# Optimization experiments

Hardware: AMD Instinct MI355X
Metric: run time of the kernel (lower is better)

Reference implementation:

```python
import jax, jax.numpy as jnp
import numpy as np

N, NC, E = 100000, 50000, 1600000   # source points, centers, edges
D, P, H, O = 64, 3, 128, 128        # feat dim, pos dim, hidden, out


def setup_inputs() -> dict:
    key = jax.random.key(0)
    ks = jax.random.split(key, 10)
    x = jax.random.normal(ks[0], (N, D), jnp.float32)
    x_c = jax.random.normal(ks[1], (NC, O), jnp.float32)  # only shape is used
    pos = jax.random.normal(ks[2], (N, P), jnp.float32)
    pos_c = jax.random.normal(ks[3], (NC, P), jnp.float32)
    src = jax.random.randint(ks[4], (E,), 0, N)
    dst = jax.random.randint(ks[5], (E,), 0, NC)
    W1 = jax.random.normal(ks[6], (D + P, H), jnp.float32) / jnp.sqrt(D + P)
    b1 = jnp.zeros((H,), jnp.float32)
    W2 = jax.random.normal(ks[7], (H, O), jnp.float32) / jnp.sqrt(H)
    b2 = jnp.zeros((O,), jnp.float32)
    return dict(x=x, x_c=x_c, pos=pos, pos_c=pos_c, src=src, dst=dst,
                W1=W1, b1=b1, W2=W2, b2=b2)


def reference(x, x_c, pos, pos_c, src, dst, W1, b1, W2, b2):
    # gather per-edge features: [E, D+P]
    feats = jnp.concatenate([x[src], pos[src] - pos_c[dst]], axis=1)
    # MLP on edges
    h = jax.nn.relu(feats @ W1 + b1) @ W2 + b2  # [E, O]
    # scatter-max aggregation onto centers
    agg = jax.ops.segment_max(h, dst, num_segments=x_c.shape[0])  # [NC, O]
    # match torch_scatter convention: empty segments -> 0 (not -inf)
    return jnp.where(jnp.isneginf(agg), 0.0, agg)
```

## Files before the change

### kernel.cpp

```cpp
#include <hip/hip_runtime.h>
#include <hip/hip_bf16.h>

#define NPTS   100000
#define NCENT  50000
#define NEDGE  1600000
#define DF     64
#define DP     3
#define DH     128
#define DOUT   128
#define TILE   128
#define LDA    104
#define LDH    136
#define LDF    66
#define NCPAD  50176

typedef __attribute__((ext_vector_type(8))) short short8;
typedef __attribute__((ext_vector_type(4))) float f32x4;

__device__ __forceinline__ unsigned short f2bf(float f) {
  union { __hip_bfloat16 h; unsigned short u; } v;
  v.h = __float2bfloat16(f);
  return v.u;
}

__device__ __forceinline__ unsigned encodeKey(float f) {
  unsigned u = __float_as_uint(f);
  return u ^ ((unsigned)((int)u >> 31) | 0x80000000u);
}

__device__ __forceinline__ float decodeKey(unsigned k) {
  if (k == 0u) return 0.0f;
  unsigned u = (k & 0x80000000u) ? (k ^ 0x80000000u) : ~k;
  return __uint_as_float(u);
}

__global__ void k_prep(const float* __restrict__ x, const float* __restrict__ W1,
                       const float* __restrict__ W2, unsigned short* __restrict__ xbf,
                       unsigned short* __restrict__ W1f, unsigned short* __restrict__ W2f,
                       int* __restrict__ cnt, unsigned* __restrict__ outU) {
  const int b = blockIdx.x;
  const int t = threadIdx.x;
  if (b < 6250) {
    int i = b * 256 + t;
    reinterpret_cast<uint4*>(outU)[i] = make_uint4(0u, 0u, 0u, 0u);
  } else if (b < 9375) {
    int i = (b - 6250) * 256 + t;
    const float4* xr = reinterpret_cast<const float4*>(x);
    float4 v0 = xr[2 * i], v1 = xr[2 * i + 1];
    short8 w;
    w[0] = (short)f2bf(v0.x); w[1] = (short)f2bf(v0.y);
    w[2] = (short)f2bf(v0.z); w[3] = (short)f2bf(v0.w);
    w[4] = (short)f2bf(v1.x); w[5] = (short)f2bf(v1.y);
    w[6] = (short)f2bf(v1.z); w[7] = (short)f2bf(v1.w);
    reinterpret_cast<short8*>(xbf)[i] = w;
  } else if (b < 9571) {
    cnt[(b - 9375) * 256 + t] = 0;
  } else if (b < 9577) {
    int tid = (b - 9571) * 256 + t;
    int lane = tid & 63, g = tid >> 6;
    int nt = g / 3, ks = g % 3;
    int n = nt * 16 + (lane & 15);
    int k0 = ks * 32 + (lane >> 4) * 8;
    short8 v;
    for (int j = 0; j < 8; ++j) {
      int k = k0 + j;
      float f = (k < DF + DP) ? W1[k * DH + n] : 0.0f;
      v[j] = (short)f2bf(f);
    }
    *reinterpret_cast<short8*>(W1f + (size_t)tid * 8) = v;
  } else {
    int tid = (b - 9577) * 256 + t;
    int lane = tid & 63, g = tid >> 6;
    int nt = g >> 2, ks = g & 3;
    int n = nt * 16 + (lane & 15);
    int k0 = ks * 32 + (lane >> 4) * 8;
    short8 v;
    for (int j = 0; j < 8; ++j) {
      int k = k0 + j;
      v[j] = (short)f2bf(W2[k * DH + n]);
    }
    *reinterpret_cast<short8*>(W2f + (size_t)tid * 8) = v;
  }
}


__global__ void k_rank(const int* __restrict__ dst, int* __restrict__ cnt,
                       int* __restrict__ rank) {
  int i = blockIdx.x * 256 + threadIdx.x;
  rank[i] = atomicAdd(&cnt[dst[i]], 1);
}

__global__ void k_s1(const int* __restrict__ cnt, int* __restrict__ bsum) {
  __shared__ int sh[256];
  int t = threadIdx.x;
  sh[t] = cnt[blockIdx.x * 256 + t];
  __syncthreads();
  for (int off = 128; off > 0; off >>= 1) {
    if (t < off) sh[t] += sh[t + off];
    __syncthreads();
  }
  if (t == 0) bsum[blockIdx.x] = sh[0];
}

__global__ void k_s2(const int* __restrict__ bsum, int* __restrict__ bbase) {
  __shared__ int sh[256];
  int t = threadIdx.x;
  int v = (t < 196) ? bsum[t] : 0;
  sh[t] = v;
  __syncthreads();
  for (int off = 1; off < 256; off <<= 1) {
    int u = (t >= off) ? sh[t - off] : 0;
    __syncthreads();
    sh[t] += u;
    __syncthreads();
  }
  if (t < 196) bbase[t] = sh[t] - v;
}

__global__ void k_s3(int* __restrict__ cnt, const int* __restrict__ bbase) {
  __shared__ int sh[256];
  int t = threadIdx.x, i = blockIdx.x * 256 + t;
  int v = cnt[i];
  sh[t] = v;
  __syncthreads();
  for (int off = 1; off < 256; off <<= 1) {
    int u = (t >= off) ? sh[t - off] : 0;
    __syncthreads();
    sh[t] += u;
    __syncthreads();
  }
  cnt[i] = sh[t] - v + bbase[blockIdx.x];
}

__global__ void k_place(const int* __restrict__ src, const int* __restrict__ dst,
                        const int* __restrict__ base, const int* __restrict__ rank,
                        unsigned long long* __restrict__ sdS) {
  int i = blockIdx.x * 256 + threadIdx.x;
  int d = dst[i];
  int p = base[d] + rank[i];
  sdS[p] = ((unsigned long long)(unsigned)d << 32) | (unsigned)src[i];
}

__global__ void k_decode(unsigned* __restrict__ out) {
  int i = blockIdx.x * blockDim.x + threadIdx.x;
  uint4 v = reinterpret_cast<uint4*>(out)[i];
  float4 f;
  f.x = decodeKey(v.x);
  f.y = decodeKey(v.y);
  f.z = decodeKey(v.z);
  f.w = decodeKey(v.w);
  reinterpret_cast<float4*>(out)[i] = f;
}

__global__ void __launch_bounds__(256, 4)
k_mlp(const unsigned short* __restrict__ xbf, const float* __restrict__ pos,
      const float* __restrict__ pos_c, const unsigned long long* __restrict__ sdS,
      const float* __restrict__ b1, const float* __restrict__ b2,
      const unsigned short* __restrict__ W1f, const unsigned short* __restrict__ W2f,
      unsigned* __restrict__ outU) {
  __shared__ __align__(16) unsigned short buf[TILE * LDH];
  __shared__ int dstLoc[TILE];

  const int t = threadIdx.x;
  const int e0 = blockIdx.x * TILE;

  {
    const int e = t >> 1, p = t & 1;
    const unsigned long long rec = sdS[e0 + e];
    const int s = (int)(rec & 0xffffffffu);
    const short8* xr = reinterpret_cast<const short8*>(xbf + (size_t)s * DF);
    for (int i = 0; i < 4; ++i)
      *reinterpret_cast<short8*>(&buf[e * LDA + p * 32 + i * 8]) = xr[p * 4 + i];
    short8 z = {0, 0, 0, 0, 0, 0, 0, 0};
    *reinterpret_cast<short8*>(&buf[e * LDA + 72 + p * 16]) = z;
    *reinterpret_cast<short8*>(&buf[e * LDA + 72 + p * 16 + 8]) = z;
  }
  if (t < TILE) {
    const unsigned long long rec = sdS[e0 + t];
    const int s = (int)(rec & 0xffffffffu);
    const int c = (int)(rec >> 32);
    dstLoc[t] = c;
    float dx = pos[(size_t)s * 3 + 0] - pos_c[(size_t)c * 3 + 0];
    float dy = pos[(size_t)s * 3 + 1] - pos_c[(size_t)c * 3 + 1];
    float dz = pos[(size_t)s * 3 + 2] - pos_c[(size_t)c * 3 + 2];
    short8 w = {0, 0, 0, 0, 0, 0, 0, 0};
    w[0] = (short)f2bf(dx); w[1] = (short)f2bf(dy); w[2] = (short)f2bf(dz);
    *reinterpret_cast<short8*>(&buf[t * LDA + 64]) = w;
  }
  __syncthreads();

  const int lane = t & 63;
  const int w = t >> 6;
  const int l16 = lane & 15;
  const int quad = lane >> 4;

  short8 a1[2][3];
  for (int mi = 0; mi < 2; ++mi) {
    int row = (2 * w + mi) * 16 + l16;
    for (int ks = 0; ks < 3; ++ks)
      a1[mi][ks] = *reinterpret_cast<const short8*>(&buf[row * LDA + ks * 32 + quad * 8]);
  }
  __syncthreads();

  for (int nt = 0; nt < 8; ++nt) {
    short8 b[3];
    for (int ks = 0; ks < 3; ++ks)
      b[ks] = *reinterpret_cast<const short8*>(W1f + ((size_t)(nt * 3 + ks) * 64 + lane) * 8);
    f32x4 acc0 = {0.f, 0.f, 0.f, 0.f}, acc1 = {0.f, 0.f, 0.f, 0.f};
    for (int ks = 0; ks < 3; ++ks) {
      acc0 = __builtin_amdgcn_mfma_f32_16x16x32_bf16(a1[0][ks], b[ks], acc0, 0, 0, 0);
      acc1 = __builtin_amdgcn_mfma_f32_16x16x32_bf16(a1[1][ks], b[ks], acc1, 0, 0, 0);
    }
    int n = nt * 16 + l16;
    float bias = b1[n];
    for (int r = 0; r < 4; ++r) {
      float v0 = acc0[r] + bias; v0 = v0 > 0.f ? v0 : 0.f;
      buf[((2 * w) * 16 + quad * 4 + r) * LDH + n] = f2bf(v0);
      float v1 = acc1[r] + bias; v1 = v1 > 0.f ? v1 : 0.f;
      buf[((2 * w + 1) * 16 + quad * 4 + r) * LDH + n] = f2bf(v1);
    }
  }
  __syncthreads();

  short8 a2[2][4];
  for (int mi = 0; mi < 2; ++mi) {
    int row = (2 * w + mi) * 16 + l16;
    for (int ks = 0; ks < 4; ++ks)
      a2[mi][ks] = *reinterpret_cast<const short8*>(&buf[row * LDH + ks * 32 + quad * 8]);
  }
  __syncthreads();

  float* Sf = reinterpret_cast<float*>(buf);
  const int col = t & 63;
  const int chunk = t >> 6;

  for (int half = 0; half < 2; ++half) {
    for (int ntl = 0; ntl < 4; ++ntl) {
      const int nt = half * 4 + ntl;
      short8 b[4];
      for (int ks = 0; ks < 4; ++ks)
        b[ks] = *reinterpret_cast<const short8*>(W2f + ((size_t)(nt * 4 + ks) * 64 + lane) * 8);
      f32x4 acc0 = {0.f, 0.f, 0.f, 0.f}, acc1 = {0.f, 0.f, 0.f, 0.f};
      for (int ks = 0; ks < 4; ++ks) {
        acc0 = __builtin_amdgcn_mfma_f32_16x16x32_bf16(a2[0][ks], b[ks], acc0, 0, 0, 0);
        acc1 = __builtin_amdgcn_mfma_f32_16x16x32_bf16(a2[1][ks], b[ks], acc1, 0, 0, 0);
      }
      const int nl = ntl * 16 + l16;
      const float bias = b2[half * 64 + nl];
      for (int r = 0; r < 4; ++r) {
        int edge0 = (2 * w) * 16 + quad * 4 + r;
        Sf[edge0 * LDF + nl] = acc0[r] + bias;
        int edge1 = (2 * w + 1) * 16 + quad * 4 + r;
        Sf[edge1 * LDF + nl] = acc1[r] + bias;
      }
    }
    __syncthreads();
    float running = -3.402823466e38f;
    int cur_d = dstLoc[chunk * 32];
    for (int i = 0; i < 32; ++i) {
      const int ei = chunk * 32 + i;
      const int d = dstLoc[ei];
      if (d != cur_d) {
        atomicMax(&outU[(size_t)cur_d * DOUT + half * 64 + col], encodeKey(running));
        running = -3.402823466e38f;
        cur_d = d;
      }
      running = fmaxf(running, Sf[ei * LDF + col]);
    }
    atomicMax(&outU[(size_t)cur_d * DOUT + half * 64 + col], encodeKey(running));
    __syncthreads();
  }
}

extern "C" void kernel_launch(void* const* d_in, const int* in_sizes, int n_in,
                              void* d_out, int out_size, void* d_ws, size_t ws_size,
                              hipStream_t stream) {
  const float* x     = (const float*)d_in[0];
  const float* pos   = (const float*)d_in[2];
  const float* pos_c = (const float*)d_in[3];
  const int*   src   = (const int*)d_in[4];
  const int*   dst   = (const int*)d_in[5];
  const float* W1    = (const float*)d_in[6];
  const float* b1    = (const float*)d_in[7];
  const float* W2    = (const float*)d_in[8];
  const float* b2    = (const float*)d_in[9];
  unsigned* outU = (unsigned*)d_out;

  char* base = (char*)d_ws;
  unsigned short* W1f = (unsigned short*)base;
  unsigned short* W2f = (unsigned short*)(base + 24576);
  int* bsum  = (int*)(base + 57344);
  int* bbase = (int*)(base + 58368);
  int* cnt   = (int*)(base + 65536);
  int* rank  = (int*)(base + 266240);
  unsigned long long* sdS = (unsigned long long*)(base + 6666240);
  unsigned short* xbf = (unsigned short*)(base + 19466240);

  k_prep<<<9585, 256, 0, stream>>>(x, W1, W2, xbf, W1f, W2f, cnt, outU);
  k_rank<<<NEDGE / 256, 256, 0, stream>>>(dst, cnt, rank);
  k_s1<<<NCPAD / 256, 256, 0, stream>>>(cnt, bsum);
  k_s2<<<1, 256, 0, stream>>>(bsum, bbase);
  k_s3<<<NCPAD / 256, 256, 0, stream>>>(cnt, bbase);
  k_place<<<NEDGE / 256, 256, 0, stream>>>(src, dst, cnt, rank, sdS);
  k_mlp<<<NEDGE / TILE, 256, 0, stream>>>(xbf, pos, pos_c, sdS,
                                          b1, b2, W1f, W2f, outU);
  k_decode<<<(NCENT * DOUT / 4) / 256, 256, 0, stream>>>(outU);
}
```

Baseline: 396.7 us.

## Drop rank array, fuse counting into prep, transpose scatter-max staging buffer

Removes the per-edge rank array by having k_place take slots with atomicAdd on the scanned offsets, and folds the dst histogram into k_prep. Zeroing of counts and output moves to hipMemsetAsync. In the MLP epilogue, results are stored transposed so each column thread reads its 32 edges as float4 vectors, and segment boundaries come from a precomputed ballot mask instead of reading dstLoc every edge. The order of edges within a segment becomes nondeterministic, which is harmless for max, and the transposed float4 LDS stores may cause bank conflicts.

```diff
diff --git a/kernel.cpp b/kernel.cpp
--- a/kernel.cpp
+++ b/kernel.cpp
@@ -11,7 +11,7 @@
 #define TILE   128
 #define LDA    104
 #define LDH    136
-#define LDF    66
+#define LDE    132
 #define NCPAD  50176
 
 typedef __attribute__((ext_vector_type(8))) short short8;
@@ -35,16 +35,13 @@
 }
 
 __global__ void k_prep(const float* __restrict__ x, const float* __restrict__ W1,
-                       const float* __restrict__ W2, unsigned short* __restrict__ xbf,
-                       unsigned short* __restrict__ W1f, unsigned short* __restrict__ W2f,
-                       int* __restrict__ cnt, unsigned* __restrict__ outU) {
+                       const float* __restrict__ W2, const int* __restrict__ dst,
+                       unsigned short* __restrict__ xbf, unsigned short* __restrict__ W1f,
+                       unsigned short* __restrict__ W2f, int* __restrict__ cnt) {
   const int b = blockIdx.x;
   const int t = threadIdx.x;
-  if (b < 6250) {
+  if (b < 3125) {
     int i = b * 256 + t;
-    reinterpret_cast<uint4*>(outU)[i] = make_uint4(0u, 0u, 0u, 0u);
-  } else if (b < 9375) {
-    int i = (b - 6250) * 256 + t;
     const float4* xr = reinterpret_cast<const float4*>(x);
     float4 v0 = xr[2 * i], v1 = xr[2 * i + 1];
     short8 w;
@@ -53,10 +50,8 @@
     w[4] = (short)f2bf(v1.x); w[5] = (short)f2bf(v1.y);
     w[6] = (short)f2bf(v1.z); w[7] = (short)f2bf(v1.w);
     reinterpret_cast<short8*>(xbf)[i] = w;
-  } else if (b < 9571) {
-    cnt[(b - 9375) * 256 + t] = 0;
-  } else if (b < 9577) {
-    int tid = (b - 9571) * 256 + t;
+  } else if (b < 3131) {
+    int tid = (b - 3125) * 256 + t;
     int lane = tid & 63, g = tid >> 6;
     int nt = g / 3, ks = g % 3;
     int n = nt * 16 + (lane & 15);
@@ -68,8 +63,8 @@
       v[j] = (short)f2bf(f);
     }
     *reinterpret_cast<short8*>(W1f + (size_t)tid * 8) = v;
-  } else {
-    int tid = (b - 9577) * 256 + t;
+  } else if (b < 3139) {
+    int tid = (b - 3131) * 256 + t;
     int lane = tid & 63, g = tid >> 6;
     int nt = g >> 2, ks = g & 3;
     int n = nt * 16 + (lane & 15);
@@ -80,15 +75,12 @@
       v[j] = (short)f2bf(W2[k * DH + n]);
     }
     *reinterpret_cast<short8*>(W2f + (size_t)tid * 8) = v;
-  }
-}
-
-
-__global__ void k_rank(const int* __restrict__ dst, int* __restrict__ cnt,
-                       int* __restrict__ rank) {
-  int i = blockIdx.x * 256 + threadIdx.x;
-  rank[i] = atomicAdd(&cnt[dst[i]], 1);
-}
+  } else {
+    int i = (b - 3139) * 256 + t;
+    atomicAdd(&cnt[dst[i]], 1);
+  }
+}
+
 
 __global__ void k_s1(const int* __restrict__ cnt, int* __restrict__ bsum) {
   __shared__ int sh[256];
@@ -133,11 +125,10 @@
 }
 
 __global__ void k_place(const int* __restrict__ src, const int* __restrict__ dst,
-                        const int* __restrict__ base, const int* __restrict__ rank,
-                        unsigned long long* __restrict__ sdS) {
+                        int* __restrict__ base, unsigned long long* __restrict__ sdS) {
   int i = blockIdx.x * 256 + threadIdx.x;
   int d = dst[i];
-  int p = base[d] + rank[i];
+  int p = atomicAdd(&base[d], 1);
   sdS[p] = ((unsigned long long)(unsigned)d << 32) | (unsigned)src[i];
 }
 
@@ -233,6 +224,14 @@
   float* Sf = reinterpret_cast<float*>(buf);
   const int col = t & 63;
   const int chunk = t >> 6;
+
+  unsigned mask32;
+  {
+    int pred = 0;
+    if (lane > 0 && lane < 32)
+      pred = (dstLoc[chunk * 32 + lane] != dstLoc[chunk * 32 + lane - 1]) ? 1 : 0;
+    mask32 = (unsigned)(__ballot(pred) & 0xffffffffull);
+  }
 
   for (int half = 0; half < 2; ++half) {
     for (int ntl = 0; ntl < 4; ++ntl) {
@@ -247,27 +246,31 @@
       }
       const int nl = ntl * 16 + l16;
       const float bias = b2[half * 64 + nl];
-      for (int r = 0; r < 4; ++r) {
-        int edge0 = (2 * w) * 16 + quad * 4 + r;
-        Sf[edge0 * LDF + nl] = acc0[r] + bias;
-        int edge1 = (2 * w + 1) * 16 + quad * 4 + r;
-        Sf[edge1 * LDF + nl] = acc1[r] + bias;
+      for (int r = 0; r < 4; ++r) { acc0[r] += bias; acc1[r] += bias; }
+      *reinterpret_cast<f32x4*>(&Sf[nl * LDE + (2 * w) * 16 + quad * 4]) = acc0;
+      *reinterpret_cast<f32x4*>(&Sf[nl * LDE + (2 * w + 1) * 16 + quad * 4]) = acc1;
+    }
+    __syncthreads();
+    float running = -3.402823466e38f;
+    const float* row = &Sf[col * LDE + chunk * 32];
+    for (int g = 0; g < 8; ++g) {
+      f32x4 v = *reinterpret_cast<const f32x4*>(row + 4 * g);
+      unsigned bits = (mask32 >> (4 * g)) & 0xFu;
+      if (bits == 0u) {
+        running = fmaxf(running, fmaxf(fmaxf(v[0], v[1]), fmaxf(v[2], v[3])));
+      } else {
+        for (int j = 0; j < 4; ++j) {
+          if ((bits >> j) & 1u) {
+            int dprev = dstLoc[chunk * 32 + 4 * g + j - 1];
+            atomicMax(&outU[(size_t)dprev * DOUT + half * 64 + col], encodeKey(running));
+            running = -3.402823466e38f;
+          }
+          running = fmaxf(running, v[j]);
+        }
       }
     }
-    __syncthreads();
-    float running = -3.402823466e38f;
-    int cur_d = dstLoc[chunk * 32];
-    for (int i = 0; i < 32; ++i) {
-      const int ei = chunk * 32 + i;
-      const int d = dstLoc[ei];
-      if (d != cur_d) {
-        atomicMax(&outU[(size_t)cur_d * DOUT + half * 64 + col], encodeKey(running));
-        running = -3.402823466e38f;
-        cur_d = d;
-      }
-      running = fmaxf(running, Sf[ei * LDF + col]);
-    }
-    atomicMax(&outU[(size_t)cur_d * DOUT + half * 64 + col], encodeKey(running));
+    int dlast = dstLoc[chunk * 32 + 31];
+    atomicMax(&outU[(size_t)dlast * DOUT + half * 64 + col], encodeKey(running));
     __syncthreads();
   }
 }
@@ -292,16 +295,16 @@
   int* bsum  = (int*)(base + 57344);
   int* bbase = (int*)(base + 58368);
   int* cnt   = (int*)(base + 65536);
-  int* rank  = (int*)(base + 266240);
-  unsigned long long* sdS = (unsigned long long*)(base + 6666240);
-  unsigned short* xbf = (unsigned short*)(base + 19466240);
-
-  k_prep<<<9585, 256, 0, stream>>>(x, W1, W2, xbf, W1f, W2f, cnt, outU);
-  k_rank<<<NEDGE / 256, 256, 0, stream>>>(dst, cnt, rank);
+  unsigned long long* sdS = (unsigned long long*)(base + 266240);
+  unsigned short* xbf = (unsigned short*)(base + 13066240);
+
+  hipMemsetAsync(cnt, 0, NCPAD * sizeof(int), stream);
+  hipMemsetAsync(outU, 0, (size_t)NCENT * DOUT * sizeof(unsigned), stream);
+  k_prep<<<9389, 256, 0, stream>>>(x, W1, W2, dst, xbf, W1f, W2f, cnt);
   k_s1<<<NCPAD / 256, 256, 0, stream>>>(cnt, bsum);
   k_s2<<<1, 256, 0, stream>>>(bsum, bbase);
   k_s3<<<NCPAD / 256, 256, 0, stream>>>(cnt, bbase);
-  k_place<<<NEDGE / 256, 256, 0, stream>>>(src, dst, cnt, rank, sdS);
+  k_place<<<NEDGE / 256, 256, 0, stream>>>(src, dst, cnt, sdS);
   k_mlp<<<NEDGE / TILE, 256, 0, stream>>>(xbf, pos, pos_c, sdS,
                                           b1, b2, W1f, W2f, outU);
   k_decode<<<(NCENT * DOUT / 4) / 256, 256, 0, stream>>>(outU);
```

Measured after the change: 475.8 us. +19.9%, slower.
